# Kernel optimization log

Hardware: AMD Instinct MI355X
Metric: run time of the kernel (lower is better)

Reference implementation:

```python
import jax, jax.numpy as jnp
import numpy as np

B, T, C = 2, 2048, 1024
H = 16
HD = C // H  # 64


def setup_inputs() -> dict:
    key = jax.random.key(0)
    k1, k2, k3, k4, k5 = jax.random.split(key, 5)
    s = 0.02
    return {
        "x": jax.random.normal(k1, (B, T, C), dtype=jnp.float32),
        "w_attn": jax.random.normal(k2, (C, 3 * C), dtype=jnp.float32) * s,
        "b_attn": jnp.zeros((3 * C,), dtype=jnp.float32),
        "w_proj": jax.random.normal(k3, (C, C), dtype=jnp.float32) * s,
        "b_proj": jnp.zeros((C,), dtype=jnp.float32),
    }


def reference(x, w_attn, b_attn, w_proj, b_proj):
    Bx, Tx, Cx = x.shape
    qkv = x @ w_attn + b_attn                      # [B,T,3C]
    q, k, v = jnp.split(qkv, 3, axis=-1)
    # [B,T,C] -> [B,H,T,HD]
    def heads(t):
        return t.reshape(Bx, Tx, H, HD).transpose(0, 2, 1, 3)
    q, k, v = heads(q), heads(k), heads(v)
    scale = 1.0 / np.sqrt(HD).astype(np.float32)
    scores = jnp.einsum("bhqd,bhkd->bhqk", q, k) * scale
    causal = jnp.tril(jnp.ones((Tx, Tx), dtype=bool))
    scores = jnp.where(causal, scores, -jnp.inf)
    attn = jax.nn.softmax(scores, axis=-1)          # dropout p=0 -> identity
    y = jnp.einsum("bhqk,bhkd->bhqd", attn, v)
    y = y.transpose(0, 2, 1, 3).reshape(Bx, Tx, Cx)
    return y @ w_proj + b_proj
```

## Files before the change

kernel.cpp:

```cpp
#include <hip/hip_runtime.h>
#include <hip/hip_bf16.h>

#define Bb 2
#define Tt 2048
#define Cc 1024
#define Hh 16
#define HD 64
#define QS 0.18033688f

typedef __attribute__((ext_vector_type(8))) short bf16x8;
typedef __attribute__((ext_vector_type(4))) short bf16x4;
typedef __attribute__((ext_vector_type(4))) float f32x4;
typedef __attribute__((ext_vector_type(2))) unsigned int u32x2;

__device__ inline short f2b(float f) {
    unsigned int u = __builtin_bit_cast(unsigned int, f);
    unsigned int r = (u + 0x7FFFu + ((u >> 16) & 1u)) >> 16;
    return (short)(unsigned short)r;
}

__device__ inline void gl16(const void* g, void* l) {
    __builtin_amdgcn_global_load_lds(
        (const __attribute__((address_space(1))) void*)g,
        (__attribute__((address_space(3))) void*)l, 16, 0, 0);
}

__global__ __launch_bounds__(256) void prep_kernel(
    const float* __restrict__ x, short* __restrict__ xbf,
    const float* __restrict__ wA, short* __restrict__ wAT,
    const float* __restrict__ wP, short* __restrict__ wPT)
{
    const int bx = blockIdx.x, tid = threadIdx.x;
    if (bx < 2048) {
        int i = (bx * 256 + tid) * 8;
        float4 a = *(const float4*)(x + i);
        float4 b = *(const float4*)(x + i + 4);
        bf16x8 v;
        v[0] = f2b(a.x); v[1] = f2b(a.y); v[2] = f2b(a.z); v[3] = f2b(a.w);
        v[4] = f2b(b.x); v[5] = f2b(b.y); v[6] = f2b(b.z); v[7] = f2b(b.w);
        *(bf16x8*)(xbf + i) = v;
        return;
    }
    const float* W; short* WT; int N, t;
    if (bx < 2816) { t = bx - 2048; W = wA; WT = wAT; N = 3072; }
    else           { t = bx - 2816; W = wP; WT = wPT; N = 1024; }
    const int K = 1024;
    int k0 = (t & 15) * 64, n0 = (t >> 4) * 64;
    int nl = tid & 63, kg = tid >> 6;
    int n = n0 + nl;
    short v[16];
#pragma unroll
    for (int i = 0; i < 16; i++)
        v[i] = f2b(W[(size_t)(k0 + kg * 16 + i) * N + n]);
    short* dst = WT + (size_t)n * K + k0 + kg * 16;
    *(bf16x8*)dst = *(bf16x8*)&v[0];
    *(bf16x8*)(dst + 8) = *(bf16x8*)&v[8];
}

#define VM0 asm volatile("s_waitcnt vmcnt(0)" ::: "memory")
#define BARRIER asm volatile("s_barrier" ::: "memory")
#define SCHEDB __builtin_amdgcn_sched_barrier(0)

#define STG(nb, kb) { \
    gl16(A + baA0 + (kb), &LB[((nb) << 1) * 4096 + dst8]); \
    gl16(A + baA0 + 32768 + (kb), &LB[((nb) << 1) * 4096 + 2048 + dst8]); \
    gl16(A + baA1 + (kb), &LB[(((nb) << 1) | 1) * 4096 + dst8]); \
    gl16(A + baA1 + 32768 + (kb), &LB[(((nb) << 1) | 1) * 4096 + 2048 + dst8]); \
    gl16(Bt + baB0 + (kb), &LB[16384 + ((nb) << 1) * 4096 + dst8]); \
    gl16(Bt + baB0 + 32768 + (kb), &LB[16384 + ((nb) << 1) * 4096 + 2048 + dst8]); \
    gl16(Bt + baB1 + (kb), &LB[16384 + (((nb) << 1) | 1) * 4096 + dst8]); \
    gl16(Bt + baB1 + 32768 + (kb), &LB[16384 + (((nb) << 1) | 1) * 4096 + 2048 + dst8]); }

#define RD_A(bb, flo) { \
    const short* Ab_ = &LB[(((bb) << 1) | wm) * 4096]; \
    _Pragma("unroll") for (int f_ = 0; f_ < 2; f_++) \
        _Pragma("unroll") for (int kh_ = 0; kh_ < 2; kh_++) \
            af[(flo) + f_][kh_] = *(const bf16x8*)&Ab_[aro[(flo) + f_] + kx[kh_]]; }

#define RD_B(bb, elo) { \
    const short* Bb_ = &LB[16384 + (((bb) << 1) | wn) * 4096]; \
    _Pragma("unroll") for (int e_ = 0; e_ < 2; e_++) \
        _Pragma("unroll") for (int kh_ = 0; kh_ < 2; kh_++) \
            bf[(elo) + e_][kh_] = *(const bf16x8*)&Bb_[bro[(elo) + e_] + kx[kh_]]; }

#define QMM(FH, EH) { \
    __builtin_amdgcn_s_setprio(1); \
    _Pragma("unroll") for (int f_ = 0; f_ < 2; f_++) \
        _Pragma("unroll") for (int e_ = 0; e_ < 2; e_++) \
            _Pragma("unroll") for (int kh_ = 0; kh_ < 2; kh_++) \
                acc[(FH) * 2 + f_][(EH) * 2 + e_] = \
                    __builtin_amdgcn_mfma_f32_16x16x32_bf16( \
                        af[(FH) * 2 + f_][kh_], bf[(EH) * 2 + e_][kh_], \
                        acc[(FH) * 2 + f_][(EH) * 2 + e_], 0, 0, 0); \
    __builtin_amdgcn_s_setprio(0); }

#define TILE(bb, nb, kb1) { \
    RD_A(bb, 0); RD_B(bb, 0); \
    STG(nb, kb1); \
    QMM(0, 0); \
    RD_B(bb, 2); QMM(0, 1); \
    RD_A(bb, 2); QMM(1, 1); \
    QMM(1, 0); \
    VM0; BARRIER; SCHEDB; }

#define TILE_LAST(bb) { \
    RD_A(bb, 0); RD_B(bb, 0); \
    QMM(0, 0); \
    RD_B(bb, 2); QMM(0, 1); \
    RD_A(bb, 2); QMM(1, 1); \
    QMM(1, 0); }

__global__ __launch_bounds__(256, 2) void gemm_qkv(
    const short* __restrict__ A, const short* __restrict__ Bt,
    const float* __restrict__ bias,
    short* __restrict__ qw, short* __restrict__ kw, short* __restrict__ vTw,
    int M, int N, int K)
{
    __shared__ __attribute__((aligned(16))) short LB[32768];

    const int tid  = threadIdx.x;
    const int wave = tid >> 6, lane = tid & 63;
    const int quad = lane >> 4, lr = lane & 15;
    const int wm = wave >> 1, wn = wave & 1;

    const int bid = blockIdx.x;
    const int sw = (bid & 7) * 96 + (bid >> 3);
    const int bx = sw % 24, by = sw / 24;
    const int m0 = by * 128, n0 = bx * 128;

    const int dst8 = tid * 8;
    const int cs = ((tid & 7) ^ ((tid >> 3) & 7)) << 3;
    const size_t baA0 = (size_t)(m0 + (tid >> 3)) * 1024 + cs;
    const size_t baA1 = (size_t)(m0 + 64 + (tid >> 3)) * 1024 + cs;
    const size_t baB0 = (size_t)(n0 + (tid >> 3)) * 1024 + cs;
    const size_t baB1 = (size_t)(n0 + 64 + (tid >> 3)) * 1024 + cs;

    int aro[4], bro[4], kx[2];
#pragma unroll
    for (int f = 0; f < 4; f++) {
        aro[f] = (f * 16 + lr) * 64;
        bro[f] = (f * 16 + lr) * 64;
    }
#pragma unroll
    for (int kh = 0; kh < 2; kh++)
        kx[kh] = (((kh * 4 + quad) ^ (lr & 7)) << 3);

    f32x4 acc[4][4];
    const f32x4 zf = {0.f, 0.f, 0.f, 0.f};
#pragma unroll
    for (int mf = 0; mf < 4; mf++)
#pragma unroll
        for (int nf = 0; nf < 4; nf++) acc[mf][nf] = zf;

    bf16x8 af[4][2], bf[4][2];

    STG(0, 0);
    VM0;
    BARRIER;

    for (int it = 0; it < 7; ++it) {
        TILE(0, 1, (2 * it + 1) << 6);
        TILE(1, 0, (2 * it + 2) << 6);
    }
    TILE(0, 1, 15 << 6);
    TILE_LAST(1);

    if (n0 < 2048) {
#pragma unroll
        for (int nf = 0; nf < 4; nf++) {
#pragma unroll
            for (int mf = 0; mf < 4; mf++) {
                int c = n0 + wn * 64 + nf * 16 + lr;
                float bv = bias[c];
#pragma unroll
                for (int r = 0; r < 4; r++) {
                    int rg = m0 + wm * 64 + mf * 16 + quad * 4 + r;
                    float val = acc[mf][nf][r] + bv;
                    int which = c >> 10, cc = c & 1023;
                    int h = cc >> 6, d = cc & 63;
                    int b = rg >> 11, t = rg & 2047;
                    size_t bh = (size_t)b * Hh + h;
                    if (which == 0) qw[(bh * Tt + t) * HD + d] = f2b(val * QS);
                    else            kw[(bh * Tt + t) * HD + d] = f2b(val);
                }
            }
        }
    } else {
        __syncthreads();
#pragma unroll
        for (int nf = 0; nf < 4; nf++) {
            int cl = wn * 64 + nf * 16 + lr;
            float bv = bias[n0 + cl];
#pragma unroll
            for (int mf = 0; mf < 4; mf++)
#pragma unroll
                for (int r = 0; r < 4; r++) {
                    int tl = wm * 64 + mf * 16 + quad * 4 + r;
                    LB[cl * 136 + tl] = f2b(acc[mf][nf][r] + bv);
                }
        }
        __syncthreads();
        const int rl = tid >> 1, half = tid & 1;
        const int cc = (n0 & 1023) + rl;
        const int h = cc >> 6, d = cc & 63;
        const int b = m0 >> 11, tb = (m0 & 2047) + half * 64;
        short* dst = vTw + (((size_t)b * Hh + h) * HD + d) * Tt + tb;
        const short* src = &LB[rl * 136 + half * 64];
#pragma unroll
        for (int jj = 0; jj < 8; jj++)
            *(bf16x8*)(dst + jj * 8) = *(const bf16x8*)(src + jj * 8);
    }
}

#define P_STG(nb, kb) { \
    gl16(A + baA0 + (size_t)(kb) * 2048, &LB[(nb) * 4096 + dst8]); \
    gl16(A + baA1 + (size_t)(kb) * 2048, &LB[(nb) * 4096 + 2048 + dst8]); \
    gl16(Bt + baB0 + (kb), &LB[8192 + (nb) * 8192 + dst8]); \
    gl16(Bt + baB1 + (kb), &LB[8192 + (nb) * 8192 + 2048 + dst8]); \
    gl16(Bt + baB2 + (kb), &LB[8192 + (nb) * 8192 + 4096 + dst8]); \
    gl16(Bt + baB3 + (kb), &LB[8192 + (nb) * 8192 + 6144 + dst8]); }

#define P_RDA(bb) { \
    const short* Ab_ = &LB[(bb) * 4096]; \
    _Pragma("unroll") for (int f_ = 0; f_ < 2; f_++) \
        _Pragma("unroll") for (int kh_ = 0; kh_ < 2; kh_++) \
            af[f_][kh_] = *(const bf16x8*)&Ab_[aro[f_] + kx[kh_]]; }

#define P_RDB(bb, elo) { \
    const short* Bb_ = &LB[8192 + (bb) * 8192]; \
    _Pragma("unroll") for (int e_ = 0; e_ < 2; e_++) \
        _Pragma("unroll") for (int kh_ = 0; kh_ < 2; kh_++) \
            bf[(elo) + e_][kh_] = *(const bf16x8*)&Bb_[bro[(elo) + e_] + kx[kh_]]; }

#define P_QMM(EH) { \
    __builtin_amdgcn_s_setprio(1); \
    _Pragma("unroll") for (int f_ = 0; f_ < 2; f_++) \
        _Pragma("unroll") for (int e_ = 0; e_ < 2; e_++) \
            _Pragma("unroll") for (int kh_ = 0; kh_ < 2; kh_++) \
                acc[f_][(EH) * 2 + e_] = \
                    __builtin_amdgcn_mfma_f32_16x16x32_bf16( \
                        af[f_][kh_], bf[(EH) * 2 + e_][kh_], \
                        acc[f_][(EH) * 2 + e_], 0, 0, 0); \
    __builtin_amdgcn_s_setprio(0); }

#define P_TILE(bb, nb, kb1) { \
    P_RDA(bb); P_RDB(bb, 0); \
    P_STG(nb, kb1); \
    P_QMM(0); \
    P_RDB(bb, 2); P_QMM(1); \
    VM0; BARRIER; SCHEDB; }

#define P_TILE_LAST(bb) { \
    P_RDA(bb); P_RDB(bb, 0); \
    P_QMM(0); \
    P_RDB(bb, 2); P_QMM(1); }

__global__ __launch_bounds__(256, 2) void gemm_proj(
    const short* __restrict__ A, const short* __restrict__ Bt,
    const float* __restrict__ bias, float* __restrict__ out,
    int M, int N, int K)
{
    __shared__ __attribute__((aligned(16))) short LB[24576];

    const int tid  = threadIdx.x;
    const int wave = tid >> 6, lane = tid & 63;
    const int quad = lane >> 4, lr = lane & 15;
    const int wm = wave >> 1, wn = wave & 1;
    const int m0 = blockIdx.y * 64, n0 = blockIdx.x * 128;

    const int dst8 = tid * 8;
    const int cs = ((tid & 7) ^ ((tid >> 3) & 7)) << 3;
    size_t baA0, baA1;
    {
        int r0 = m0 + (tid >> 3), r1 = m0 + 32 + (tid >> 3);
        baA0 = (((size_t)(r0 >> 11) * Hh) * Tt + (r0 & 2047)) * HD + cs;
        baA1 = (((size_t)(r1 >> 11) * Hh) * Tt + (r1 & 2047)) * HD + cs;
    }
    const size_t baB0 = (size_t)(n0 + (tid >> 3)) * 1024 + cs;
    const size_t baB1 = (size_t)(n0 + 32 + (tid >> 3)) * 1024 + cs;
    const size_t baB2 = (size_t)(n0 + 64 + (tid >> 3)) * 1024 + cs;
    const size_t baB3 = (size_t)(n0 + 96 + (tid >> 3)) * 1024 + cs;

    int aro[2], bro[4], kx[2];
#pragma unroll
    for (int f = 0; f < 2; f++) aro[f] = (wm * 32 + f * 16 + lr) * 64;
#pragma unroll
    for (int e = 0; e < 4; e++) bro[e] = (wn * 64 + e * 16 + lr) * 64;
#pragma unroll
    for (int kh = 0; kh < 2; kh++)
        kx[kh] = (((kh * 4 + quad) ^ (lr & 7)) << 3);

    f32x4 acc[2][4];
    const f32x4 zf = {0.f, 0.f, 0.f, 0.f};
#pragma unroll
    for (int mi = 0; mi < 2; mi++)
#pragma unroll
        for (int ni = 0; ni < 4; ni++) acc[mi][ni] = zf;

    bf16x8 af[2][2], bf[4][2];

    P_STG(0, 0);
    VM0;
    BARRIER;

    for (int it = 0; it < 7; ++it) {
        P_TILE(0, 1, (2 * it + 1) << 6);
        P_TILE(1, 0, (2 * it + 2) << 6);
    }
    P_TILE(0, 1, 15 << 6);
    P_TILE_LAST(1);

#pragma unroll
    for (int mi = 0; mi < 2; mi++)
#pragma unroll
        for (int ni = 0; ni < 4; ni++) {
            int c = n0 + wn * 64 + ni * 16 + lr;
            float bv = bias[c];
#pragma unroll
            for (int r = 0; r < 4; r++) {
                int rg = m0 + wm * 32 + mi * 16 + quad * 4 + r;
                out[(size_t)rg * N + c] = acc[mi][ni][r] + bv;
            }
        }
}

__global__ __launch_bounds__(256) void gemm_f32src(
    const void* __restrict__ Araw, const float* __restrict__ Bm,
    const float* __restrict__ bias, float* __restrict__ out,
    short* __restrict__ qw, short* __restrict__ kw, short* __restrict__ vTw,
    int M, int N, int K, int mode)
{
    __shared__ __attribute__((aligned(16))) short As[128 * 32];
    __shared__ __attribute__((aligned(16))) short Bs[128 * 32];

    const int tid  = threadIdx.x;
    const int wave = tid >> 6, lane = tid & 63;
    const int quad = lane >> 4, lr = lane & 15;
    const int wm = wave >> 1, wn = wave & 1;
    const int m0 = blockIdx.y * 128, n0 = blockIdx.x * 128;

    f32x4 acc[4][4];
    const f32x4 zf = {0.f, 0.f, 0.f, 0.f};
#pragma unroll
    for (int mi = 0; mi < 4; mi++)
#pragma unroll
        for (int ni = 0; ni < 4; ni++) acc[mi][ni] = zf;

    for (int k0 = 0; k0 < K; k0 += 32) {
        __syncthreads();
        if (mode == 1) {
            const float* Af = (const float*)Araw;
#pragma unroll
            for (int i = 0; i < 4; i++) {
                int id  = i * 256 + tid;
                int row = id >> 3;
                int kc  = (id & 7) << 2;
                float4 v = *(const float4*)(Af + (size_t)(m0 + row) * K + k0 + kc);
                short* d = &As[row * 32 + kc];
                d[0] = f2b(v.x); d[1] = f2b(v.y); d[2] = f2b(v.z); d[3] = f2b(v.w);
            }
        } else {
            const short* Ah = (const short*)Araw;
#pragma unroll
            for (int i = 0; i < 2; i++) {
                int id  = i * 256 + tid;
                int row = id >> 2;
                int kc  = (id & 3) << 3;
                int rg = m0 + row, b = rg >> 11, t = rg & 2047;
                int c = k0 + kc, h = c >> 6, d = c & 63;
                *(bf16x8*)&As[row * 32 + kc] =
                    *(const bf16x8*)(Ah + ((((size_t)b * Hh + h) * Tt + t) * HD + d));
            }
        }
#pragma unroll
        for (int i = 0; i < 4; i++) {
            int id = i * 256 + tid;
            int kr = id >> 5;
            int nc = (id & 31) << 2;
            float4 v = *(const float4*)(Bm + (size_t)(k0 + kr) * N + n0 + nc);
            Bs[(nc + 0) * 32 + kr] = f2b(v.x);
            Bs[(nc + 1) * 32 + kr] = f2b(v.y);
            Bs[(nc + 2) * 32 + kr] = f2b(v.z);
            Bs[(nc + 3) * 32 + kr] = f2b(v.w);
        }
        __syncthreads();

        bf16x8 af[4], bf[4];
#pragma unroll
        for (int mi = 0; mi < 4; mi++)
            af[mi] = *(bf16x8*)&As[(wm * 64 + mi * 16 + lr) * 32 + quad * 8];
#pragma unroll
        for (int ni = 0; ni < 4; ni++)
            bf[ni] = *(bf16x8*)&Bs[(wn * 64 + ni * 16 + lr) * 32 + quad * 8];
#pragma unroll
        for (int mi = 0; mi < 4; mi++)
#pragma unroll
            for (int ni = 0; ni < 4; ni++)
                acc[mi][ni] = __builtin_amdgcn_mfma_f32_16x16x32_bf16(
                    af[mi], bf[ni], acc[mi][ni], 0, 0, 0);
    }

#pragma unroll
    for (int mi = 0; mi < 4; mi++) {
#pragma unroll
        for (int ni = 0; ni < 4; ni++) {
            int c = n0 + wn * 64 + ni * 16 + lr;
            float bv = bias[c];
#pragma unroll
            for (int r = 0; r < 4; r++) {
                int rg = m0 + wm * 64 + mi * 16 + quad * 4 + r;
                float val = acc[mi][ni][r] + bv;
                if (mode == 1) {
                    int which = c >> 10, cc = c & 1023;
                    int h = cc >> 6, d = cc & 63;
                    int b = rg >> 11, t = rg & 2047;
                    size_t bh = (size_t)b * Hh + h;
                    if (which == 0)      qw[(bh * Tt + t) * HD + d] = f2b(val * QS);
                    else if (which == 1) kw[(bh * Tt + t) * HD + d] = f2b(val);
                    else                 vTw[(bh * HD + d) * Tt + t] = f2b(val);
                } else {
                    out[(size_t)rg * N + c] = val;
                }
            }
        }
    }
}

__global__ __launch_bounds__(512) void attn_kernel(
    short* __restrict__ qw, const short* __restrict__ kw,
    const short* __restrict__ vTw)
{
    __shared__ __attribute__((aligned(16))) short Ks[2][8192];
    __shared__ __attribute__((aligned(16))) short Vs[2][8192];

    const int bh = blockIdx.x & 31;
    const int g  = blockIdx.x >> 5;
    const int tid = threadIdx.x;
    const int wave = tid >> 6, lane = tid & 63;
    const int wg = wave & 3, kgrp = wave >> 2;
    const int quad = lane >> 4, lr = lane & 15;

    const int pA = 2 * g + (wg >> 1);
    const int pB = 63 - pA;
    const int wh = (wg & 1) * 16;
    const int r0m[2] = { pA * 32 + wh, pB * 32 + wh };

    short* qp = qw + (size_t)bh * Tt * HD;
    const short* kp = kw + (size_t)bh * Tt * HD;
    const short* vp = vTw + (size_t)bh * HD * Tt;

    int krow[2], kcol[2], vrow[2], vcol[2];
#pragma unroll
    for (int i = 0; i < 2; i++) {
        int id = i * 512 + tid;
        krow[i] = id >> 3;
        kcol[i] = ((id & 7) ^ (krow[i] & 7)) << 3;
        vrow[i] = id >> 4;
        vcol[i] = ((id & 15) ^ (vrow[i] & 15)) << 3;
    }

    const int kb0b = lr * 64 + ((quad     ^ (lr & 7)) << 3);
    const int kb1b = lr * 64 + (((4 + quad) ^ (lr & 7)) << 3);
    const int qh = quad >> 1, ql = quad & 1;
    int vbase[4];
#pragma unroll
    for (int nt = 0; nt < 4; nt++)
        vbase[nt] = (nt * 16 + lr) * 128 + ql * 4;

    bf16x8 aq[2][2];
#pragma unroll
    for (int mt = 0; mt < 2; mt++)
#pragma unroll
        for (int h = 0; h < 2; h++)
            aq[mt][h] = *(const bf16x8*)(qp + (size_t)(r0m[mt] + lr) * HD
                                            + h * 32 + quad * 8);

    const f32x4 zf = {0.f, 0.f, 0.f, 0.f};
    f32x4 o[2][4];
    float lacc[2] = {0.f, 0.f};
#pragma unroll
    for (int mt = 0; mt < 2; mt++)
#pragma unroll
        for (int nt = 0; nt < 4; nt++) o[mt][nt] = zf;

#pragma unroll
    for (int i = 0; i < 2; i++) {
        gl16(kp + (size_t)krow[i] * HD + kcol[i], &Ks[0][(i * 512 + tid) * 8]);
        gl16(vp + (size_t)vrow[i] * Tt + vcol[i], &Vs[0][(i * 512 + tid) * 8]);
    }

    const int clast = ((63 - 2 * g) * 32 + 31) >> 7;
    for (int c = 0; c <= clast; ++c) {
        const int j0 = c << 7;
        const int cur = c & 1;
        __syncthreads();
        if (c < clast) {
#pragma unroll
            for (int i = 0; i < 2; i++) {
                gl16(kp + (size_t)(j0 + 128 + krow[i]) * HD + kcol[i],
                     &Ks[cur ^ 1][(i * 512 + tid) * 8]);
                gl16(vp + (size_t)vrow[i] * Tt + (j0 + 128) + vcol[i],
                     &Vs[cur ^ 1][(i * 512 + tid) * 8]);
            }
        }
        const short* Kc = &Ks[cur][0];
        const short* Vc = &Vs[cur][0];
        __builtin_amdgcn_s_setprio(1);
#pragma unroll
        for (int k4 = 0; k4 < 4; k4++) {
            const int kt = kgrp * 4 + k4;
            const int k16 = j0 + kt * 16;
            const bool act0 = k16 <= r0m[0] + 15;
            const bool act1 = k16 <= r0m[1] + 15;
            if (!act1 && !act0) break;
            bf16x8 kb0 = *(const bf16x8*)&Kc[kt * 1024 + kb0b];
            bf16x8 kb1 = *(const bf16x8*)&Kc[kt * 1024 + kb1b];
            const int sl8 = (((kt * 2 + qh) ^ lr) << 3);
            bf16x4 va[4];
#pragma unroll
            for (int nt = 0; nt < 4; nt++)
                va[nt] = *(const bf16x4*)&Vc[vbase[nt] + sl8];
#pragma unroll
            for (int mt = 0; mt < 2; mt++) {
                if (!(mt ? act1 : act0)) continue;
                f32x4 s = __builtin_amdgcn_mfma_f32_16x16x32_bf16(
                    kb0, aq[mt][0], zf, 0, 0, 0);
                s = __builtin_amdgcn_mfma_f32_16x16x32_bf16(
                    kb1, aq[mt][1], s, 0, 0, 0);
                unsigned u[4];
                if (k16 + 15 <= r0m[mt]) {
#pragma unroll
                    for (int r = 0; r < 4; r++) {
                        float e = __builtin_amdgcn_exp2f(s[r]);
                        u[r] = __builtin_bit_cast(unsigned, e);
                        lacc[mt] += e;
                    }
                } else {
#pragma unroll
                    for (int r = 0; r < 4; r++) {
                        float e = __builtin_amdgcn_exp2f(s[r]);
                        if ((k16 + quad * 4 + r) > (r0m[mt] + lr)) e = 0.f;
                        u[r] = __builtin_bit_cast(unsigned, e);
                        lacc[mt] += e;
                    }
                }
                u32x2 pu = { __builtin_amdgcn_perm(u[1], u[0], 0x07060302u),
                             __builtin_amdgcn_perm(u[3], u[2], 0x07060302u) };
                bf16x4 pt = __builtin_bit_cast(bf16x4, pu);
#pragma unroll
                for (int nt = 0; nt < 4; nt++)
                    o[mt][nt] = __builtin_amdgcn_mfma_f32_16x16x16bf16_1k(
                        va[nt], pt, o[mt][nt], 0, 0, 0);
            }
        }
        __builtin_amdgcn_s_setprio(0);
    }

    __syncthreads();
    float* po = (float*)&Ks[0][0];
    float* pl = (float*)&Vs[0][0];
    if (kgrp) {
#pragma unroll
        for (int mt = 0; mt < 2; mt++)
#pragma unroll
            for (int nt = 0; nt < 4; nt++)
                *(f32x4*)&po[(wg * 64 + lane) * 32 + (mt * 4 + nt) * 4] = o[mt][nt];
        pl[(wg * 64 + lane) * 2 + 0] = lacc[0];
        pl[(wg * 64 + lane) * 2 + 1] = lacc[1];
    }
    __syncthreads();
    if (kgrp == 0) {
#pragma unroll
        for (int mt = 0; mt < 2; mt++)
#pragma unroll
            for (int nt = 0; nt < 4; nt++) {
                f32x4 t = *(const f32x4*)&po[(wg * 64 + lane) * 32 + (mt * 4 + nt) * 4];
#pragma unroll
                for (int r = 0; r < 4; r++) o[mt][nt][r] += t[r];
            }
        lacc[0] += pl[(wg * 64 + lane) * 2 + 0];
        lacc[1] += pl[(wg * 64 + lane) * 2 + 1];

#pragma unroll
        for (int mt = 0; mt < 2; mt++) {
            lacc[mt] += __shfl_xor(lacc[mt], 16, 64);
            lacc[mt] += __shfl_xor(lacc[mt], 32, 64);
            lacc[mt] = 1.0f / lacc[mt];
        }

#pragma unroll
        for (int mt = 0; mt < 2; mt++)
#pragma unroll
            for (int nt = 0; nt < 4; nt++) {
                bf16x4 ov;
#pragma unroll
                for (int r = 0; r < 4; r++) ov[r] = f2b(o[mt][nt][r] * lacc[mt]);
                *(bf16x4*)(qp + (size_t)(r0m[mt] + lr) * HD + nt * 16 + quad * 4) = ov;
            }
    }
}

extern "C" void kernel_launch(void* const* d_in, const int* in_sizes, int n_in,
                              void* d_out, int out_size, void* d_ws, size_t ws_size,
                              hipStream_t stream) {
    const float* x      = (const float*)d_in[0];
    const float* w_attn = (const float*)d_in[1];
    const float* b_attn = (const float*)d_in[2];
    const float* w_proj = (const float*)d_in[3];
    const float* b_proj = (const float*)d_in[4];
    float* out = (float*)d_out;

    const size_t per = (size_t)Bb * Hh * Tt * HD;
    short* qw  = (short*)d_ws;
    short* kw  = qw + per;
    short* vTw = kw + per;
    const int M = Bb * Tt;

    const size_t need_fast = (3 * per + per + (size_t)3072 * 1024 + (size_t)1024 * 1024) * 2;

    if (ws_size >= need_fast) {
        short* xbf = vTw + per;
        short* wAT = xbf + per;
        short* wPT = wAT + (size_t)3072 * 1024;

        prep_kernel<<<dim3(3072), 256, 0, stream>>>(x, xbf, w_attn, wAT, w_proj, wPT);

        gemm_qkv<<<dim3(768), 256, 0, stream>>>(
            xbf, wAT, b_attn, qw, kw, vTw, M, 3 * Cc, Cc);

        attn_kernel<<<dim3(512), 512, 0, stream>>>(qw, kw, vTw);

        gemm_proj<<<dim3(Cc / 128, M / 64), 256, 0, stream>>>(
            qw, wPT, b_proj, out, M, Cc, Cc);
    } else {
        gemm_f32src<<<dim3(3 * Cc / 128, M / 128), 256, 0, stream>>>(
            x, w_attn, b_attn, nullptr, qw, kw, vTw, M, 3 * Cc, Cc, 1);

        attn_kernel<<<dim3(512), 512, 0, stream>>>(qw, kw, vTw);

        gemm_f32src<<<dim3(Cc / 128, M / 128), 256, 0, stream>>>(
            qw, w_proj, b_proj, out, nullptr, nullptr, nullptr, M, Cc, Cc, 2);
    }
}
```

Measured before the change: 171.5 us.

## Halve QKV GEMM K-tile to 32 to cut LDS and raise occupancy to 3

The QKV projection GEMM now stages 32-wide K slices instead of 64-wide ones. That shrinks shared memory from 64KB to about 34KB and the fragment registers from 8 to 4 per operand, and launch bounds rise to 3 blocks per CU. The swizzle and read offsets are reworked for the narrower tile, and the loop runs twice as many iterations with one wait and barrier each. The intent is more resident blocks to hide memory latency. In exchange there are twice as many barriers and less MFMA work between them.

```diff
diff --git a/kernel.cpp b/kernel.cpp
--- a/kernel.cpp
+++ b/kernel.cpp
@@ -61,62 +61,38 @@
 #define BARRIER asm volatile("s_barrier" ::: "memory")
 #define SCHEDB __builtin_amdgcn_sched_barrier(0)
 
-#define STG(nb, kb) { \
-    gl16(A + baA0 + (kb), &LB[((nb) << 1) * 4096 + dst8]); \
-    gl16(A + baA0 + 32768 + (kb), &LB[((nb) << 1) * 4096 + 2048 + dst8]); \
-    gl16(A + baA1 + (kb), &LB[(((nb) << 1) | 1) * 4096 + dst8]); \
-    gl16(A + baA1 + 32768 + (kb), &LB[(((nb) << 1) | 1) * 4096 + 2048 + dst8]); \
-    gl16(Bt + baB0 + (kb), &LB[16384 + ((nb) << 1) * 4096 + dst8]); \
-    gl16(Bt + baB0 + 32768 + (kb), &LB[16384 + ((nb) << 1) * 4096 + 2048 + dst8]); \
-    gl16(Bt + baB1 + (kb), &LB[16384 + (((nb) << 1) | 1) * 4096 + dst8]); \
-    gl16(Bt + baB1 + 32768 + (kb), &LB[16384 + (((nb) << 1) | 1) * 4096 + 2048 + dst8]); }
-
-#define RD_A(bb, flo) { \
-    const short* Ab_ = &LB[(((bb) << 1) | wm) * 4096]; \
-    _Pragma("unroll") for (int f_ = 0; f_ < 2; f_++) \
-        _Pragma("unroll") for (int kh_ = 0; kh_ < 2; kh_++) \
-            af[(flo) + f_][kh_] = *(const bf16x8*)&Ab_[aro[(flo) + f_] + kx[kh_]]; }
-
-#define RD_B(bb, elo) { \
-    const short* Bb_ = &LB[16384 + (((bb) << 1) | wn) * 4096]; \
-    _Pragma("unroll") for (int e_ = 0; e_ < 2; e_++) \
-        _Pragma("unroll") for (int kh_ = 0; kh_ < 2; kh_++) \
-            bf[(elo) + e_][kh_] = *(const bf16x8*)&Bb_[bro[(elo) + e_] + kx[kh_]]; }
-
-#define QMM(FH, EH) { \
+#define Q_STG(nb, kb) { \
+    gl16(A + baA0 + (kb), &LB[(nb) * 4096 + dst8]); \
+    gl16(A + baA1 + (kb), &LB[(nb) * 4096 + 2048 + dst8]); \
+    gl16(Bt + baB0 + (kb), &LB[8192 + (nb) * 4096 + dst8]); \
+    gl16(Bt + baB1 + (kb), &LB[8192 + (nb) * 4096 + 2048 + dst8]); }
+
+#define Q_RD(bb) { \
+    const short* Ab_ = &LB[(bb) * 4096]; \
+    const short* Bb_ = &LB[8192 + (bb) * 4096]; \
+    _Pragma("unroll") for (int f_ = 0; f_ < 4; f_++) \
+        af[f_] = *(const bf16x8*)&Ab_[aro[f_] + kxs]; \
+    _Pragma("unroll") for (int e_ = 0; e_ < 4; e_++) \
+        bf[e_] = *(const bf16x8*)&Bb_[bro[e_] + kxs]; }
+
+#define Q_MM { \
     __builtin_amdgcn_s_setprio(1); \
-    _Pragma("unroll") for (int f_ = 0; f_ < 2; f_++) \
-        _Pragma("unroll") for (int e_ = 0; e_ < 2; e_++) \
-            _Pragma("unroll") for (int kh_ = 0; kh_ < 2; kh_++) \
-                acc[(FH) * 2 + f_][(EH) * 2 + e_] = \
-                    __builtin_amdgcn_mfma_f32_16x16x32_bf16( \
-                        af[(FH) * 2 + f_][kh_], bf[(EH) * 2 + e_][kh_], \
-                        acc[(FH) * 2 + f_][(EH) * 2 + e_], 0, 0, 0); \
+    _Pragma("unroll") for (int f_ = 0; f_ < 4; f_++) \
+        _Pragma("unroll") for (int e_ = 0; e_ < 4; e_++) \
+            acc[f_][e_] = __builtin_amdgcn_mfma_f32_16x16x32_bf16( \
+                af[f_], bf[e_], acc[f_][e_], 0, 0, 0); \
     __builtin_amdgcn_s_setprio(0); }
 
-#define TILE(bb, nb, kb1) { \
-    RD_A(bb, 0); RD_B(bb, 0); \
-    STG(nb, kb1); \
-    QMM(0, 0); \
-    RD_B(bb, 2); QMM(0, 1); \
-    RD_A(bb, 2); QMM(1, 1); \
-    QMM(1, 0); \
-    VM0; BARRIER; SCHEDB; }
-
-#define TILE_LAST(bb) { \
-    RD_A(bb, 0); RD_B(bb, 0); \
-    QMM(0, 0); \
-    RD_B(bb, 2); QMM(0, 1); \
-    RD_A(bb, 2); QMM(1, 1); \
-    QMM(1, 0); }
-
-__global__ __launch_bounds__(256, 2) void gemm_qkv(
+#define Q_TILE(bb, nb, kb1) { Q_RD(bb); Q_STG(nb, kb1); Q_MM; VM0; BARRIER; SCHEDB; }
+#define Q_TILE_LAST(bb)     { Q_RD(bb); Q_MM; }
+
+__global__ __launch_bounds__(256, 3) void gemm_qkv(
     const short* __restrict__ A, const short* __restrict__ Bt,
     const float* __restrict__ bias,
     short* __restrict__ qw, short* __restrict__ kw, short* __restrict__ vTw,
     int M, int N, int K)
 {
-    __shared__ __attribute__((aligned(16))) short LB[32768];
+    __shared__ __attribute__((aligned(16))) short LB[17408];
 
     const int tid  = threadIdx.x;
     const int wave = tid >> 6, lane = tid & 63;
@@ -129,21 +105,20 @@
     const int m0 = by * 128, n0 = bx * 128;
 
     const int dst8 = tid * 8;
-    const int cs = ((tid & 7) ^ ((tid >> 3) & 7)) << 3;
-    const size_t baA0 = (size_t)(m0 + (tid >> 3)) * 1024 + cs;
-    const size_t baA1 = (size_t)(m0 + 64 + (tid >> 3)) * 1024 + cs;
-    const size_t baB0 = (size_t)(n0 + (tid >> 3)) * 1024 + cs;
-    const size_t baB1 = (size_t)(n0 + 64 + (tid >> 3)) * 1024 + cs;
-
-    int aro[4], bro[4], kx[2];
+    const int cs = ((tid & 3) ^ ((tid >> 4) & 3)) << 3;
+    const int r = tid >> 2;
+    const size_t baA0 = (size_t)(m0 + r) * 1024 + cs;
+    const size_t baA1 = (size_t)(m0 + 64 + r) * 1024 + cs;
+    const size_t baB0 = (size_t)(n0 + r) * 1024 + cs;
+    const size_t baB1 = (size_t)(n0 + 64 + r) * 1024 + cs;
+
+    int aro[4], bro[4];
 #pragma unroll
     for (int f = 0; f < 4; f++) {
-        aro[f] = (f * 16 + lr) * 64;
-        bro[f] = (f * 16 + lr) * 64;
-    }
-#pragma unroll
-    for (int kh = 0; kh < 2; kh++)
-        kx[kh] = (((kh * 4 + quad) ^ (lr & 7)) << 3);
+        aro[f] = (wm * 64 + f * 16 + lr) * 32;
+        bro[f] = (wn * 64 + f * 16 + lr) * 32;
+    }
+    const int kxs = ((quad ^ ((lr >> 2) & 3)) << 3);
 
     f32x4 acc[4][4];
     const f32x4 zf = {0.f, 0.f, 0.f, 0.f};
@@ -152,18 +127,18 @@
 #pragma unroll
         for (int nf = 0; nf < 4; nf++) acc[mf][nf] = zf;
 
-    bf16x8 af[4][2], bf[4][2];
-
-    STG(0, 0);
+    bf16x8 af[4], bf[4];
+
+    Q_STG(0, 0);
     VM0;
     BARRIER;
 
-    for (int it = 0; it < 7; ++it) {
-        TILE(0, 1, (2 * it + 1) << 6);
-        TILE(1, 0, (2 * it + 2) << 6);
-    }
-    TILE(0, 1, 15 << 6);
-    TILE_LAST(1);
+    for (int it = 0; it < 15; ++it) {
+        Q_TILE(0, 1, (2 * it + 1) << 5);
+        Q_TILE(1, 0, (2 * it + 2) << 5);
+    }
+    Q_TILE(0, 1, 31 << 5);
+    Q_TILE_LAST(1);
 
     if (n0 < 2048) {
 #pragma unroll
@@ -173,9 +148,9 @@
                 int c = n0 + wn * 64 + nf * 16 + lr;
                 float bv = bias[c];
 #pragma unroll
-                for (int r = 0; r < 4; r++) {
-                    int rg = m0 + wm * 64 + mf * 16 + quad * 4 + r;
-                    float val = acc[mf][nf][r] + bv;
+                for (int r2 = 0; r2 < 4; r2++) {
+                    int rg = m0 + wm * 64 + mf * 16 + quad * 4 + r2;
+                    float val = acc[mf][nf][r2] + bv;
                     int which = c >> 10, cc = c & 1023;
                     int h = cc >> 6, d = cc & 63;
                     int b = rg >> 11, t = rg & 2047;
@@ -194,9 +169,9 @@
 #pragma unroll
             for (int mf = 0; mf < 4; mf++)
 #pragma unroll
-                for (int r = 0; r < 4; r++) {
-                    int tl = wm * 64 + mf * 16 + quad * 4 + r;
-                    LB[cl * 136 + tl] = f2b(acc[mf][nf][r] + bv);
+                for (int r2 = 0; r2 < 4; r2++) {
+                    int tl = wm * 64 + mf * 16 + quad * 4 + r2;
+                    LB[cl * 136 + tl] = f2b(acc[mf][nf][r2] + bv);
                 }
         }
         __syncthreads();
@@ -317,9 +292,9 @@
             int c = n0 + wn * 64 + ni * 16 + lr;
             float bv = bias[c];
 #pragma unroll
-            for (int r = 0; r < 4; r++) {
-                int rg = m0 + wm * 32 + mi * 16 + quad * 4 + r;
-                out[(size_t)rg * N + c] = acc[mi][ni][r] + bv;
+            for (int r2 = 0; r2 < 4; r2++) {
+                int rg = m0 + wm * 32 + mi * 16 + quad * 4 + r2;
+                out[(size_t)rg * N + c] = acc[mi][ni][r2] + bv;
             }
         }
 }
```

Measured after the change: 175.2 us. +2.2%, slower.
